# Kernel tuning notes

Measured on AMD Instinct MI355X. Metric: run time of the kernel, lower is better.

## Reference

```python
import jax, jax.numpy as jnp
import numpy as np

N, E = 50000, 800000
MUL, NATTR, NEMB, HID, NPATH = 32, 8, 8, 8, 5
AVG_NEIGH = 16.0
INV3 = 1.0 / np.sqrt(3.0)  # CG norm for 1o x 1o -> 0e (dot)
INV2 = 1.0 / np.sqrt(2.0)  # CG norm for 1o x 1o -> 1o (cross)


def setup_inputs() -> dict:
    key = jax.random.key(0)
    ks = jax.random.split(key, 16)
    f = lambda k, s: jax.random.normal(k, s, jnp.float32)
    return {
        "node_s": f(ks[0], (N, MUL)),
        "node_v": f(ks[1], (N, MUL, 3)),
        "node_attrs": f(ks[2], (N, NATTR)),
        "edge_emb": f(ks[3], (E, NEMB)),
        "edge_sh0": f(ks[4], (E, 1)),
        "edge_sh1": f(ks[5], (E, 3)),
        "W1_s": f(ks[6], (MUL, MUL)),
        "W1_v": f(ks[7], (MUL, MUL)),
        "Wm1": f(ks[8], (NEMB, HID)),
        "Wm2": f(ks[9], (HID, NPATH * MUL)),
        "W2_s": f(ks[10], (2 * MUL, MUL)),
        "W2_v": f(ks[11], (3 * MUL, MUL)),
        "Wsc_s": f(ks[12], (MUL, NATTR, MUL)),
        "Wsc_v": f(ks[13], (MUL, NATTR, MUL)),
        "edge_src": jax.random.randint(ks[14], (E,), 0, N),
        "edge_dst": jax.random.randint(ks[15], (E,), 0, N),
    }


def reference(node_s, node_v, node_attrs, edge_emb, edge_sh0, edge_sh1,
              W1_s, W1_v, Wm1, Wm2, W2_s, W2_v, Wsc_s, Wsc_v,
              edge_src, edge_dst):
    # linear_1: per-l equivariant channel mixing
    x_s = node_s @ W1_s / np.sqrt(MUL)                          # [N, MUL]
    x_v = jnp.einsum('nuc,uv->nvc', node_v, W1_v) / np.sqrt(MUL)  # [N, MUL, 3]
    # gather source node features per edge
    s = x_s[edge_src]   # [E, MUL]
    v = x_v[edge_src]   # [E, MUL, 3]
    # radial MLP on edge embedding -> per-edge UVU tensor-product weights
    h = jax.nn.silu(edge_emb @ Wm1 / np.sqrt(NEMB))
    w = (h @ Wm2 / np.sqrt(HID)).reshape(E, NPATH, MUL)
    w1, w2, w3, w4, w5 = (w[:, i] for i in range(NPATH))
    # UVU Clebsch-Gordan paths (lmax = 1)
    p1 = w1 * s * edge_sh0                                              # 0e x 0e -> 0e
    p2 = w2 * jnp.einsum('euc,ec->eu', v, edge_sh1) * INV3              # 1o x 1o -> 0e
    p3 = w3[:, :, None] * s[:, :, None] * edge_sh1[:, None, :]          # 0e x 1o -> 1o
    p4 = w4[:, :, None] * v * edge_sh0[:, :, None]                      # 1o x 0e -> 1o
    p5 = w5[:, :, None] * jnp.cross(v, edge_sh1[:, None, :]) * INV2     # 1o x 1o -> 1o
    msg_s = jnp.concatenate([p1, p2], axis=1)       # [E, 2*MUL]
    msg_v = jnp.concatenate([p3, p4, p5], axis=1)   # [E, 3*MUL, 3]
    # scatter-add messages to destination nodes
    agg_s = jax.ops.segment_sum(msg_s, edge_dst, num_segments=N)
    agg_v = jax.ops.segment_sum(msg_v, edge_dst, num_segments=N)
    inv = 1.0 / np.sqrt(AVG_NEIGH)
    agg_s = agg_s * inv
    agg_v = agg_v * inv
    # linear_2
    m_s = agg_s @ W2_s / np.sqrt(2 * MUL)
    m_v = jnp.einsum('nuc,uv->nvc', agg_v, W2_v) / np.sqrt(3 * MUL)
    # self connection: fully connected TP with scalar node attrs
    nsc = 1.0 / np.sqrt(MUL * NATTR)
    sc_s = jnp.einsum('nu,na,uav->nv', node_s, node_attrs, Wsc_s) * nsc
    sc_v = jnp.einsum('nuc,na,uav->nvc', node_v, node_attrs, Wsc_v) * nsc
    out_s = m_s + sc_s                  # [N, MUL]
    out_v = m_v + sc_v                  # [N, MUL, 3]
    return jnp.concatenate([out_s, out_v.reshape(N, MUL * 3)], axis=1)  # [N, 128]
```

## Files before the change

### kernel.cpp

```cpp
#include <hip/hip_runtime.h>
#include <math.h>

#define NN 50000
#define NE 800000
#define MUL 32
#define CHUNK 16
#define SCANB 49

static __device__ __forceinline__ float sigmoidf_(float v) {
    return 1.0f / (1.0f + __expf(-v));
}

#define INV_SQRT_MUL   0.17677669529663687f
#define INV_SQRT_NEMB  0.35355339059327373f
#define INV_SQRT_HID   0.35355339059327373f
#define INV3C          0.5773502691896258f
#define INV2C          0.7071067811865476f
#define INV_NEIGH      0.25f
#define INV_SQRT_2MUL  0.125f
#define INV_SQRT_3MUL  0.10206207261596575f
#define NSC            0.0625f

__global__ __launch_bounds__(256) void k_node(
    const float* __restrict__ node_s, const float* __restrict__ node_v,
    const float* __restrict__ attrs,
    const float* __restrict__ W1_s, const float* __restrict__ W1_v,
    const float* __restrict__ Wsc_s, const float* __restrict__ Wsc_v,
    float* __restrict__ x, float* __restrict__ out)
{
    __shared__ float nd[2][136];
    __shared__ float gs[2][1024];
    __shared__ float gv[2][1024];
    const int t  = threadIdx.x;
    const int h  = t >> 7;
    const int tl = t & 127;
    const int n  = blockIdx.x * 2 + h;

    if (tl < 32) nd[h][tl] = node_s[n * 32 + tl];
    else         nd[h][tl] = node_v[n * 96 + (tl - 32)];
    if (tl < 8)  nd[h][128 + tl] = attrs[n * 8 + tl];
    __syncthreads();

    float at[8];
#pragma unroll
    for (int a = 0; a < 8; ++a) at[a] = nd[h][128 + a];

#pragma unroll
    for (int r = 0; r < 8; ++r) {
        int idx = tl + 128 * r;
        int u = idx >> 5, vch = idx & 31;
        float as = 0.f, av = 0.f;
#pragma unroll
        for (int a = 0; a < 8; ++a) {
            as += at[a] * Wsc_s[(u * 8 + a) * 32 + vch];
            av += at[a] * Wsc_v[(u * 8 + a) * 32 + vch];
        }
        gs[h][idx] = as;
        gv[h][idx] = av;
    }
    __syncthreads();

    float xa = 0.f, sc = 0.f;
    if (tl < 32) {
#pragma unroll
        for (int u = 0; u < 32; ++u) {
            xa += nd[h][u] * W1_s[u * 32 + tl];
            sc += nd[h][u] * gs[h][(u << 5) + tl];
        }
    } else {
        int q = tl - 32;
        int vch = q / 3, c = q - 3 * vch;
#pragma unroll
        for (int u = 0; u < 32; ++u) {
            float vv = nd[h][32 + u * 3 + c];
            xa += vv * W1_v[u * 32 + vch];
            sc += vv * gv[h][(u << 5) + vch];
        }
    }
    x[n * 128 + tl]   = xa * INV_SQRT_MUL;
    out[n * 128 + tl] = sc * NSC;
}

__global__ __launch_bounds__(256) void k_hist(
    const int* __restrict__ edge_dst, int* __restrict__ counts)
{
    int e = blockIdx.x * 256 + threadIdx.x;
    if (e >= NE) return;
    atomicAdd(&counts[edge_dst[e]], 1);
}

__global__ __launch_bounds__(1024) void k_scan_a(
    const int* __restrict__ counts, int* __restrict__ escan,
    int* __restrict__ bsum)
{
    __shared__ int sh[1024];
    const int t = threadIdx.x;
    const int i = blockIdx.x * 1024 + t;
    int v = (i < NN) ? counts[i] : 0;
    sh[t] = v;
    __syncthreads();
    for (int off = 1; off < 1024; off <<= 1) {
        int u = (t >= off) ? sh[t - off] : 0;
        __syncthreads();
        sh[t] += u;
        __syncthreads();
    }
    if (i < NN) escan[i] = sh[t] - v;
    if (t == 1023) bsum[blockIdx.x] = sh[1023];
}

__global__ __launch_bounds__(64) void k_scan_b(int* __restrict__ bsum)
{
    const int t = threadIdx.x;
    int v = (t < SCANB) ? bsum[t] : 0;
    const int orig = v;
    for (int off = 1; off < 64; off <<= 1) {
        int u = __shfl_up(v, off, 64);
        if (t >= off) v += u;
    }
    if (t < SCANB) bsum[t] = v - orig;
}

__global__ __launch_bounds__(1024) void k_scan_c(
    const int* __restrict__ escan, const int* __restrict__ bsum,
    int* __restrict__ offsets, int* __restrict__ cursor)
{
    const int i = blockIdx.x * 1024 + threadIdx.x;
    if (i == 0) offsets[NN] = NE;
    if (i < NN) {
        int o = bsum[blockIdx.x] + escan[i];
        offsets[i] = o;
        cursor[i] = o;
    }
}

__global__ __launch_bounds__(256) void k_pack(
    const float* __restrict__ edge_emb, const float* __restrict__ edge_sh0,
    const float* __restrict__ edge_sh1,
    const int* __restrict__ edge_src, const int* __restrict__ edge_dst,
    const float* __restrict__ Wm1,
    int* __restrict__ cursor, float* __restrict__ epack)
{
    int e = blockIdx.x * 256 + threadIdx.x;
    if (e >= NE) return;
    const float4* p = (const float4*)(edge_emb + e * 8);
    float4 a = p[0], b = p[1];
    float emb[8] = {a.x, a.y, a.z, a.w, b.x, b.y, b.z, b.w};
    float h[8];
#pragma unroll
    for (int j = 0; j < 8; ++j) {
        float s = 0.f;
#pragma unroll
        for (int k = 0; k < 8; ++k) s += emb[k] * Wm1[k * 8 + j];
        s *= INV_SQRT_NEMB;
        h[j] = s * sigmoidf_(s);
    }
    float sh0 = edge_sh0[e];
    float sx = edge_sh1[3 * e], sy = edge_sh1[3 * e + 1], sz = edge_sh1[3 * e + 2];
    int src = edge_src[e];
    int pos = atomicAdd(&cursor[edge_dst[e]], 1);
    float4* op = (float4*)(epack + (size_t)pos * 16);
    op[0] = make_float4(__int_as_float(src), sh0, sx, sy);
    op[1] = make_float4(sz, h[0], h[1], h[2]);
    op[2] = make_float4(h[3], h[4], h[5], h[6]);
    op[3] = make_float4(h[7], 0.f, 0.f, 0.f);
}

__global__ __launch_bounds__(64) void k_gather(
    const float* __restrict__ x, const float* __restrict__ epack,
    const float* __restrict__ Wm2, const float* __restrict__ W2_s,
    const float* __restrict__ W2_v,
    const int* __restrict__ offsets, float* __restrict__ out)
{
    __shared__ float meta[CHUNK * 16];
    __shared__ float msg[352];
    const int n = blockIdx.x;
    const int L = threadIdx.x;
    const int u = L & 31;
    const int role = L >> 5;

    float wc[3][8];
#pragma unroll
    for (int p = 0; p < 3; ++p) {
        int m = (role == 0 ? p : 3 + p) * 32 + u;
        if (m > 159) m = u;
#pragma unroll
        for (int q = 0; q < 8; ++q) wc[p][q] = Wm2[q * 160 + m];
    }

    float a0 = 0.f, a1 = 0.f;
    float b0 = 0.f, b1 = 0.f, b2 = 0.f;
    float c0 = 0.f, c1 = 0.f, c2 = 0.f;

    const int beg = offsets[n];
    const int end = offsets[n + 1];

    for (int base = beg; base < end; base += CHUNK) {
        const int cnt = min(CHUNK, end - base);
        {
            int ee = L >> 2;
            if (ee < cnt) {
                float4 v = ((const float4*)epack)[(size_t)(base + ee) * 4 + (L & 3)];
                *(float4*)&meta[ee * 16 + 4 * (L & 3)] = v;
            }
        }
        __syncthreads();

        float ls, lv0, lv1, lv2;
        {
            const float* xr = x + (size_t)__float_as_int(meta[0]) * 128;
            ls  = xr[u];
            lv0 = xr[32 + 3 * u]; lv1 = xr[33 + 3 * u]; lv2 = xr[34 + 3 * u];
        }
        for (int jj = 0; jj < cnt; ++jj) {
            float ns = 0.f, nv0 = 0.f, nv1 = 0.f, nv2 = 0.f;
            if (jj + 1 < cnt) {
                const float* xr = x + (size_t)__float_as_int(meta[(jj + 1) * 16]) * 128;
                ns  = xr[u];
                nv0 = xr[32 + 3 * u]; nv1 = xr[33 + 3 * u]; nv2 = xr[34 + 3 * u];
            }
            const float* mp = &meta[jj * 16];
            const float sh0 = mp[1], sx = mp[2], sy = mp[3], sz = mp[4];
            float w0 = 0.f, w1 = 0.f, w2 = 0.f;
#pragma unroll
            for (int q = 0; q < 8; ++q) {
                float hq = mp[5 + q];
                w0 += hq * wc[0][q];
                w1 += hq * wc[1][q];
                w2 += hq * wc[2][q];
            }
            w0 *= INV_SQRT_HID; w1 *= INV_SQRT_HID; w2 *= INV_SQRT_HID;
            if (role == 0) {
                a0 += w0 * ls * sh0;
                float dot = lv0 * sx + lv1 * sy + lv2 * sz;
                a1 += w1 * dot;
                float t = w2 * ls;
                b0 += t * sx; b1 += t * sy; b2 += t * sz;
            } else {
                float t4 = w0 * sh0;
                b0 += t4 * lv0; b1 += t4 * lv1; b2 += t4 * lv2;
                float cx = lv1 * sz - lv2 * sy;
                float cy = lv2 * sx - lv0 * sz;
                float cz = lv0 * sy - lv1 * sx;
                c0 += w1 * cx; c1 += w1 * cy; c2 += w1 * cz;
            }
            ls = ns; lv0 = nv0; lv1 = nv1; lv2 = nv2;
        }
        __syncthreads();
    }

    if (role == 0) {
        msg[u]      = a0 * INV_NEIGH;
        msg[32 + u] = a1 * (INV3C * INV_NEIGH);
        int vb = 64 + u * 3;
        msg[vb]     = b0 * INV_NEIGH;
        msg[vb + 1] = b1 * INV_NEIGH;
        msg[vb + 2] = b2 * INV_NEIGH;
    } else {
        int vb4 = 64 + (32 + u) * 3;
        msg[vb4]     = b0 * INV_NEIGH;
        msg[vb4 + 1] = b1 * INV_NEIGH;
        msg[vb4 + 2] = b2 * INV_NEIGH;
        int vb5 = 64 + (64 + u) * 3;
        float f = INV2C * INV_NEIGH;
        msg[vb5]     = c0 * f;
        msg[vb5 + 1] = c1 * f;
        msg[vb5 + 2] = c2 * f;
    }
    __syncthreads();

#pragma unroll
    for (int oo = 0; oo < 2; ++oo) {
        int o = oo * 64 + L;
        float r;
        if (o < 32) {
            float s = 0.f;
#pragma unroll
            for (int uu = 0; uu < 64; ++uu) s += msg[uu] * W2_s[uu * 32 + o];
            r = s * INV_SQRT_2MUL;
        } else {
            int q = o - 32;
            int vch = q / 3, c = q - 3 * vch;
            float s = 0.f;
#pragma unroll
            for (int uu = 0; uu < 96; ++uu) s += msg[64 + uu * 3 + c] * W2_v[uu * 32 + vch];
            r = s * INV_SQRT_3MUL;
        }
        out[128 * n + o] += r;
    }
}

extern "C" void kernel_launch(void* const* d_in, const int* in_sizes, int n_in,
                              void* d_out, int out_size, void* d_ws, size_t ws_size,
                              hipStream_t stream) {
    const float* node_s   = (const float*)d_in[0];
    const float* node_v   = (const float*)d_in[1];
    const float* attrs    = (const float*)d_in[2];
    const float* edge_emb = (const float*)d_in[3];
    const float* edge_sh0 = (const float*)d_in[4];
    const float* edge_sh1 = (const float*)d_in[5];
    const float* W1_s     = (const float*)d_in[6];
    const float* W1_v     = (const float*)d_in[7];
    const float* Wm1      = (const float*)d_in[8];
    const float* Wm2      = (const float*)d_in[9];
    const float* W2_s     = (const float*)d_in[10];
    const float* W2_v     = (const float*)d_in[11];
    const float* Wsc_s    = (const float*)d_in[12];
    const float* Wsc_v    = (const float*)d_in[13];
    const int*   edge_src = (const int*)d_in[14];
    const int*   edge_dst = (const int*)d_in[15];
    float* out = (float*)d_out;

    float* x     = (float*)d_ws;
    float* epack = x + (size_t)NN * 128;
    int*   counts  = (int*)(epack + (size_t)NE * 16);
    int*   offsets = counts + NN;
    int*   cursor  = offsets + NN + 1;
    int*   escan   = cursor + NN;
    int*   bsum    = escan + NN;

    hipMemsetAsync(counts, 0, NN * sizeof(int), stream);

    k_node<<<NN / 2, 256, 0, stream>>>(node_s, node_v, attrs,
                                       W1_s, W1_v, Wsc_s, Wsc_v, x, out);
    k_hist<<<(NE + 255) / 256, 256, 0, stream>>>(edge_dst, counts);
    k_scan_a<<<SCANB, 1024, 0, stream>>>(counts, escan, bsum);
    k_scan_b<<<1, 64, 0, stream>>>(bsum);
    k_scan_c<<<SCANB, 1024, 0, stream>>>(escan, bsum, offsets, cursor);
    k_pack<<<(NE + 255) / 256, 256, 0, stream>>>(edge_emb, edge_sh0, edge_sh1,
                                                 edge_src, edge_dst, Wm1,
                                                 cursor, epack);
    k_gather<<<NN, 64, 0, stream>>>(x, epack, Wm2, W2_s, W2_v, offsets, out);
}
```

Before: 498.1 us.

## Fuse histogram into node kernel, merge scan stages, repack x for float4 gathers

The edge histogram atomics move into the node-transform kernel, which now handles four nodes per block (12500 blocks × 256 threads covers all 800000 edges). The separate block-sum scan kernel is dropped; each scan_c block reduces the preceding block sums itself. The transformed node features x are stored interleaved as [s, vx, vy, vz] per channel, so the gather kernel fetches each source row with one float4 load. The gather loop also drops the shared-memory chunk staging and its barriers in favour of register prefetch of the next edge record. This cuts launches and barrier and latency overhead, at the cost of a larger shared-memory footprint per node-kernel block and a changed layout for x.

```diff
diff --git a/kernel.cpp b/kernel.cpp
--- a/kernel.cpp
+++ b/kernel.cpp
@@ -4,7 +4,7 @@
 #define NN 50000
 #define NE 800000
 #define MUL 32
-#define CHUNK 16
+#define NPB 4
 #define SCANB 49
 
 static __device__ __forceinline__ float sigmoidf_(float v) {
@@ -26,67 +26,102 @@
     const float* __restrict__ attrs,
     const float* __restrict__ W1_s, const float* __restrict__ W1_v,
     const float* __restrict__ Wsc_s, const float* __restrict__ Wsc_v,
+    const int* __restrict__ edge_dst, int* __restrict__ counts,
     float* __restrict__ x, float* __restrict__ out)
 {
-    __shared__ float nd[2][136];
-    __shared__ float gs[2][1024];
-    __shared__ float gv[2][1024];
+    __shared__ float nd[NPB][136];
+    __shared__ float gs[NPB][1024];
+    __shared__ float gv[NPB][1024];
     const int t  = threadIdx.x;
-    const int h  = t >> 7;
-    const int tl = t & 127;
-    const int n  = blockIdx.x * 2 + h;
-
-    if (tl < 32) nd[h][tl] = node_s[n * 32 + tl];
-    else         nd[h][tl] = node_v[n * 96 + (tl - 32)];
-    if (tl < 8)  nd[h][128 + tl] = attrs[n * 8 + tl];
-    __syncthreads();
-
-    float at[8];
-#pragma unroll
-    for (int a = 0; a < 8; ++a) at[a] = nd[h][128 + a];
-
-#pragma unroll
-    for (int r = 0; r < 8; ++r) {
-        int idx = tl + 128 * r;
-        int u = idx >> 5, vch = idx & 31;
-        float as = 0.f, av = 0.f;
+    const int nb = blockIdx.x * NPB;
+
+    {
+        int g = blockIdx.x * 256 + t;
+        if (g < NE) atomicAdd(&counts[edge_dst[g]], 1);
+    }
+
+#pragma unroll
+    for (int i = t; i < NPB * 128; i += 256) {
+        int nn = i >> 7, j = i & 127;
+        nd[nn][j] = (j < 32) ? node_s[(nb + nn) * 32 + j]
+                             : node_v[(nb + nn) * 96 + (j - 32)];
+    }
+    if (t < NPB * 8) nd[t >> 3][128 + (t & 7)] = attrs[(nb + (t >> 3)) * 8 + (t & 7)];
+    __syncthreads();
+
+    float at[NPB][8];
+#pragma unroll
+    for (int nn = 0; nn < NPB; ++nn)
+#pragma unroll
+        for (int a = 0; a < 8; ++a) at[nn][a] = nd[nn][128 + a];
+
+#pragma unroll
+    for (int r = 0; r < 4; ++r) {
+        const int idx = t + 256 * r;
+        const int u = idx >> 5, vch = idx & 31;
+        float as[NPB] = {0.f, 0.f, 0.f, 0.f};
+        float av[NPB] = {0.f, 0.f, 0.f, 0.f};
 #pragma unroll
         for (int a = 0; a < 8; ++a) {
-            as += at[a] * Wsc_s[(u * 8 + a) * 32 + vch];
-            av += at[a] * Wsc_v[(u * 8 + a) * 32 + vch];
-        }
-        gs[h][idx] = as;
-        gv[h][idx] = av;
-    }
-    __syncthreads();
-
-    float xa = 0.f, sc = 0.f;
-    if (tl < 32) {
-#pragma unroll
-        for (int u = 0; u < 32; ++u) {
-            xa += nd[h][u] * W1_s[u * 32 + tl];
-            sc += nd[h][u] * gs[h][(u << 5) + tl];
+            const float ws = Wsc_s[(u * 8 + a) * 32 + vch];
+            const float wv = Wsc_v[(u * 8 + a) * 32 + vch];
+#pragma unroll
+            for (int nn = 0; nn < NPB; ++nn) {
+                as[nn] += at[nn][a] * ws;
+                av[nn] += at[nn][a] * wv;
+            }
+        }
+#pragma unroll
+        for (int nn = 0; nn < NPB; ++nn) {
+            gs[nn][idx] = as[nn];
+            gv[nn][idx] = av[nn];
+        }
+    }
+    __syncthreads();
+
+    const int o  = t & 127;
+    const int nh = t >> 7;
+    if (o < 32) {
+        float ax[2] = {0.f, 0.f}, asc[2] = {0.f, 0.f};
+#pragma unroll
+        for (int uu = 0; uu < 32; ++uu) {
+            const float w1 = W1_s[uu * 32 + o];
+#pragma unroll
+            for (int r2 = 0; r2 < 2; ++r2) {
+                const int nn = nh + 2 * r2;
+                const float s = nd[nn][uu];
+                ax[r2]  += s * w1;
+                asc[r2] += s * gs[nn][(uu << 5) + o];
+            }
+        }
+#pragma unroll
+        for (int r2 = 0; r2 < 2; ++r2) {
+            const int nidx = nb + nh + 2 * r2;
+            x[(size_t)nidx * 128 + 4 * o] = ax[r2] * INV_SQRT_MUL;
+            out[(size_t)nidx * 128 + o]   = asc[r2] * NSC;
         }
     } else {
-        int q = tl - 32;
-        int vch = q / 3, c = q - 3 * vch;
-#pragma unroll
-        for (int u = 0; u < 32; ++u) {
-            float vv = nd[h][32 + u * 3 + c];
-            xa += vv * W1_v[u * 32 + vch];
-            sc += vv * gv[h][(u << 5) + vch];
-        }
-    }
-    x[n * 128 + tl]   = xa * INV_SQRT_MUL;
-    out[n * 128 + tl] = sc * NSC;
-}
-
-__global__ __launch_bounds__(256) void k_hist(
-    const int* __restrict__ edge_dst, int* __restrict__ counts)
-{
-    int e = blockIdx.x * 256 + threadIdx.x;
-    if (e >= NE) return;
-    atomicAdd(&counts[edge_dst[e]], 1);
+        const int q = o - 32;
+        const int vch = q / 3, c = q - 3 * vch;
+        float ax[2] = {0.f, 0.f}, asc[2] = {0.f, 0.f};
+#pragma unroll
+        for (int uu = 0; uu < 32; ++uu) {
+            const float w1 = W1_v[uu * 32 + vch];
+#pragma unroll
+            for (int r2 = 0; r2 < 2; ++r2) {
+                const int nn = nh + 2 * r2;
+                const float vv = nd[nn][32 + 3 * uu + c];
+                ax[r2]  += vv * w1;
+                asc[r2] += vv * gv[nn][(uu << 5) + vch];
+            }
+        }
+#pragma unroll
+        for (int r2 = 0; r2 < 2; ++r2) {
+            const int nidx = nb + nh + 2 * r2;
+            x[(size_t)nidx * 128 + 4 * vch + 1 + c] = ax[r2] * INV_SQRT_MUL;
+            out[(size_t)nidx * 128 + o]             = asc[r2] * NSC;
+        }
+    }
 }
 
 __global__ __launch_bounds__(1024) void k_scan_a(
@@ -109,26 +144,22 @@
     if (t == 1023) bsum[blockIdx.x] = sh[1023];
 }
 
-__global__ __launch_bounds__(64) void k_scan_b(int* __restrict__ bsum)
-{
-    const int t = threadIdx.x;
-    int v = (t < SCANB) ? bsum[t] : 0;
-    const int orig = v;
-    for (int off = 1; off < 64; off <<= 1) {
-        int u = __shfl_up(v, off, 64);
-        if (t >= off) v += u;
-    }
-    if (t < SCANB) bsum[t] = v - orig;
-}
-
 __global__ __launch_bounds__(1024) void k_scan_c(
     const int* __restrict__ escan, const int* __restrict__ bsum,
     int* __restrict__ offsets, int* __restrict__ cursor)
 {
-    const int i = blockIdx.x * 1024 + threadIdx.x;
+    __shared__ int sbase;
+    const int t = threadIdx.x;
+    if (t < 64) {
+        int v = (t < blockIdx.x) ? bsum[t] : 0;
+        for (int off = 32; off > 0; off >>= 1) v += __shfl_xor(v, off, 64);
+        if (t == 0) sbase = v;
+    }
+    __syncthreads();
+    const int i = blockIdx.x * 1024 + t;
     if (i == 0) offsets[NN] = NE;
     if (i < NN) {
-        int o = bsum[blockIdx.x] + escan[i];
+        int o = sbase + escan[i];
         offsets[i] = o;
         cursor[i] = o;
     }
@@ -172,7 +203,6 @@
     const float* __restrict__ W2_v,
     const int* __restrict__ offsets, float* __restrict__ out)
 {
-    __shared__ float meta[CHUNK * 16];
     __shared__ float msg[352];
     const int n = blockIdx.x;
     const int L = threadIdx.x;
@@ -195,58 +225,51 @@
     const int beg = offsets[n];
     const int end = offsets[n + 1];
 
-    for (int base = beg; base < end; base += CHUNK) {
-        const int cnt = min(CHUNK, end - base);
-        {
-            int ee = L >> 2;
-            if (ee < cnt) {
-                float4 v = ((const float4*)epack)[(size_t)(base + ee) * 4 + (L & 3)];
-                *(float4*)&meta[ee * 16 + 4 * (L & 3)] = v;
-            }
-        }
-        __syncthreads();
-
-        float ls, lv0, lv1, lv2;
-        {
-            const float* xr = x + (size_t)__float_as_int(meta[0]) * 128;
-            ls  = xr[u];
-            lv0 = xr[32 + 3 * u]; lv1 = xr[33 + 3 * u]; lv2 = xr[34 + 3 * u];
-        }
-        for (int jj = 0; jj < cnt; ++jj) {
-            float ns = 0.f, nv0 = 0.f, nv1 = 0.f, nv2 = 0.f;
-            if (jj + 1 < cnt) {
-                const float* xr = x + (size_t)__float_as_int(meta[(jj + 1) * 16]) * 128;
-                ns  = xr[u];
-                nv0 = xr[32 + 3 * u]; nv1 = xr[33 + 3 * u]; nv2 = xr[34 + 3 * u];
-            }
-            const float* mp = &meta[jj * 16];
-            const float sh0 = mp[1], sx = mp[2], sy = mp[3], sz = mp[4];
-            float w0 = 0.f, w1 = 0.f, w2 = 0.f;
-#pragma unroll
-            for (int q = 0; q < 8; ++q) {
-                float hq = mp[5 + q];
-                w0 += hq * wc[0][q];
-                w1 += hq * wc[1][q];
-                w2 += hq * wc[2][q];
-            }
+    if (end > beg) {
+        const float4* rp = (const float4*)(epack + (size_t)beg * 16);
+        float4 r0 = rp[0];
+        float4 r1 = rp[1];
+        float4 r2 = rp[2];
+        float  h7 = epack[(size_t)beg * 16 + 12];
+        float4 xv = *(const float4*)(x + (size_t)__float_as_int(r0.x) * 128 + 4 * u);
+
+        for (int e = beg; e < end; ++e) {
+            const int ip = (e + 1 < end) ? (e + 1) : e;
+            const float4* np = (const float4*)(epack + (size_t)ip * 16);
+            const float4 q0 = np[0];
+            const float4 q1 = np[1];
+            const float4 q2 = np[2];
+            const float  qh7 = epack[(size_t)ip * 16 + 12];
+            const float4 nxv = *(const float4*)(x + (size_t)__float_as_int(q0.x) * 128 + 4 * u);
+
+            const float sh0 = r0.y, sx = r0.z, sy = r0.w, sz = r1.x;
+            float w0 = r1.y * wc[0][0] + r1.z * wc[0][1] + r1.w * wc[0][2]
+                     + r2.x * wc[0][3] + r2.y * wc[0][4] + r2.z * wc[0][5]
+                     + r2.w * wc[0][6] + h7  * wc[0][7];
+            float w1 = r1.y * wc[1][0] + r1.z * wc[1][1] + r1.w * wc[1][2]
+                     + r2.x * wc[1][3] + r2.y * wc[1][4] + r2.z * wc[1][5]
+                     + r2.w * wc[1][6] + h7  * wc[1][7];
+            float w2 = r1.y * wc[2][0] + r1.z * wc[2][1] + r1.w * wc[2][2]
+                     + r2.x * wc[2][3] + r2.y * wc[2][4] + r2.z * wc[2][5]
+                     + r2.w * wc[2][6] + h7  * wc[2][7];
             w0 *= INV_SQRT_HID; w1 *= INV_SQRT_HID; w2 *= INV_SQRT_HID;
+
+            const float ls = xv.x, lv0 = xv.y, lv1 = xv.z, lv2 = xv.w;
             if (role == 0) {
                 a0 += w0 * ls * sh0;
-                float dot = lv0 * sx + lv1 * sy + lv2 * sz;
-                a1 += w1 * dot;
-                float t = w2 * ls;
-                b0 += t * sx; b1 += t * sy; b2 += t * sz;
+                a1 += w1 * (lv0 * sx + lv1 * sy + lv2 * sz);
+                float tt = w2 * ls;
+                b0 += tt * sx; b1 += tt * sy; b2 += tt * sz;
             } else {
                 float t4 = w0 * sh0;
                 b0 += t4 * lv0; b1 += t4 * lv1; b2 += t4 * lv2;
-                float cx = lv1 * sz - lv2 * sy;
-                float cy = lv2 * sx - lv0 * sz;
-                float cz = lv0 * sy - lv1 * sx;
-                c0 += w1 * cx; c1 += w1 * cy; c2 += w1 * cz;
+                c0 += w1 * (lv1 * sz - lv2 * sy);
+                c1 += w1 * (lv2 * sx - lv0 * sz);
+                c2 += w1 * (lv0 * sy - lv1 * sx);
             }
-            ls = ns; lv0 = nv0; lv1 = nv1; lv2 = nv2;
-        }
-        __syncthreads();
+            r0 = q0; r1 = q1; r2 = q2; h7 = qh7;
+            xv = nxv;
+        }
     }
 
     if (role == 0) {
@@ -321,11 +344,10 @@
 
     hipMemsetAsync(counts, 0, NN * sizeof(int), stream);
 
-    k_node<<<NN / 2, 256, 0, stream>>>(node_s, node_v, attrs,
-                                       W1_s, W1_v, Wsc_s, Wsc_v, x, out);
-    k_hist<<<(NE + 255) / 256, 256, 0, stream>>>(edge_dst, counts);
+    k_node<<<NN / NPB, 256, 0, stream>>>(node_s, node_v, attrs,
+                                         W1_s, W1_v, Wsc_s, Wsc_v,
+                                         edge_dst, counts, x, out);
     k_scan_a<<<SCANB, 1024, 0, stream>>>(counts, escan, bsum);
-    k_scan_b<<<1, 64, 0, stream>>>(bsum);
     k_scan_c<<<SCANB, 1024, 0, stream>>>(escan, bsum, offsets, cursor);
     k_pack<<<(NE + 255) / 256, 256, 0, stream>>>(edge_emb, edge_sh0, edge_sh1,
                                                  edge_src, edge_dst, Wm1,
```

Measured after the change: 416.9 us. 16.3% less time.
